# Kernel optimization log

Hardware: AMD Instinct MI355X
Metric: run time of the kernel (lower is better)

The kernel has to match this reference:

```python
import jax, jax.numpy as jnp
import numpy as np

B, H, W, C, WS, NCLS = 8, 256, 256, 256, 8, 18


def setup_inputs() -> dict:
    key = jax.random.key(0)
    ks = jax.random.split(key, 10)
    s = 1.0 / np.sqrt(C)
    return {
        "x": jax.random.normal(ks[0], (B, H, W, C), jnp.float32),
        "Wq": jax.random.normal(ks[1], (C, NCLS), jnp.float32) * s,
        "bq": jnp.zeros((NCLS,), jnp.float32),
        "Wk": jax.random.normal(ks[2], (C, NCLS), jnp.float32) * s,
        "bk": jnp.zeros((NCLS,), jnp.float32),
        "Wv": jax.random.normal(ks[3], (C, C), jnp.float32) * s,
        "bv": jnp.zeros((C,), jnp.float32),
        "Wres": jax.random.normal(ks[4], (C, C), jnp.float32) * s,
        "bres": jnp.zeros((C,), jnp.float32),
        "gamma": jnp.zeros((1,), jnp.float32) + 0.1,
    }


def _window_partition(x):
    # (B,H,W,C) -> (B*nH*nW, ws*ws, C)
    b, h, w, c = x.shape
    x = x.reshape(b, h // WS, WS, w // WS, WS, c)
    x = jnp.transpose(x, (0, 1, 3, 2, 4, 5))
    return x.reshape(-1, WS * WS, c)


def _window_reverse(xw, c):
    # (B*nH*nW, ws*ws, c) -> (B,H,W,c)
    x = xw.reshape(B, H // WS, W // WS, WS, WS, c)
    x = jnp.transpose(x, (0, 1, 3, 2, 4, 5))
    return x.reshape(B, H, W, c)


def reference(x, Wq, bq, Wk, bk, Wv, bv, Wres, bres, gamma):
    xw = _window_partition(x)                      # (nWin, ws^2, C)
    seg_map = xw @ Wq + bq                         # (nWin, ws^2, n_cls)
    seg_ft = xw @ Wk + bk                          # (nWin, ws^2, n_cls)
    feats = xw @ Wv + bv                           # (nWin, ws^2, C)
    score = jnp.einsum('nik,njk->nij', seg_map, seg_ft)  # (nWin, ws^2, ws^2)
    score = jax.nn.softmax(score, axis=-1)
    feats = jnp.einsum('nij,njc->nic', score, feats)
    feats = feats @ Wres + bres                    # dropout = identity (eval)
    feat_map = gamma * feats + xw
    return _window_reverse(seg_map, NCLS), _window_reverse(feat_map, C)
```

## Files before the change

### kernel.cpp

```cpp
#include <hip/hip_runtime.h>
#include <hip/hip_bf16.h>


typedef __bf16 bf16_t;
typedef __bf16 bf16x8 __attribute__((ext_vector_type(8)));
typedef __bf16 bf16x4 __attribute__((ext_vector_type(4)));
typedef float  f32x4  __attribute__((ext_vector_type(4)));

#define MFMA16(a, b, c) __builtin_amdgcn_mfma_f32_16x16x32_bf16((a), (b), (c), 0, 0, 0)

static constexpr int kC = 256, kNCLS = 18;
static constexpr int WQT_OFF = 0;
static constexpr int WKT_OFF = 8192;
static constexpr int WFT_OFF = 16384;
static constexpr int BF_BYTE_OFF = 81920 * 2;

__global__ __launch_bounds__(256) void prep_kernel(
    const float* __restrict__ Wq, const float* __restrict__ Wk,
    const float* __restrict__ Wv, const float* __restrict__ bv,
    const float* __restrict__ Wres, const float* __restrict__ bres,
    bf16_t* __restrict__ wsb, float* __restrict__ bff)
{
  const int blk = blockIdx.x, t = threadIdx.x;
  if (blk < 256) {
    __shared__ float wcol[256];
    const int n = blk;
    wcol[t] = Wres[t * kC + n];
    __syncthreads();
    float acc = 0.f;
    const float* wvrow = Wv + (size_t)t * kC;
#pragma unroll 4
    for (int j = 0; j < 256; j += 4) {
      f32x4 a = *(const f32x4*)(wvrow + j);
      acc += a[0] * wcol[j] + a[1] * wcol[j + 1] + a[2] * wcol[j + 2] + a[3] * wcol[j + 3];
    }
    wsb[WFT_OFF + n * kC + t] = (bf16_t)acc;
  } else if (blk == 256) {
    float acc = bres[t];
    for (int j = 0; j < 256; ++j) acc += bv[j] * Wres[j * kC + t];
    bff[t] = acc;
  } else {
    int tid = (blk - 257) * 256 + t;
    if (tid < 8192) {
      int n = tid >> 8, k = tid & 255;
      wsb[WQT_OFF + tid] = (n < kNCLS) ? (bf16_t)Wq[k * kNCLS + n] : (bf16_t)0.0f;
    } else {
      int u = tid - 8192;
      int n = u >> 8, k = u & 255;
      wsb[WKT_OFF + u] = (n < kNCLS) ? (bf16_t)Wk[k * kNCLS + n] : (bf16_t)0.0f;
    }
  }
}

__global__ __launch_bounds__(256, 3) void semwin_main(
    const float* __restrict__ x,
    const float* __restrict__ bq, const float* __restrict__ bk,
    const float* __restrict__ gamma,
    const bf16_t* __restrict__ wsb, const float* __restrict__ bff,
    float* __restrict__ out0, float* __restrict__ out1)
{
  __shared__ bf16_t xs[64][264];
  __shared__ __align__(16) char buf1[10240];
  __shared__ __align__(16) char buf2[9216];

  bf16_t (* const Qs)[40]  = (bf16_t(*)[40])(buf1);
  bf16_t (* const Ks)[40]  = (bf16_t(*)[40])(buf1 + 5120);
  bf16_t (* const Ps)[72]  = (bf16_t(*)[72])(buf1);
  bf16_t (* const Utc)[72] = (bf16_t(*)[72])(buf2);

  const int tid  = threadIdx.x;
  const int wave = tid >> 6;
  const int lane = tid & 63;
  const int l15  = lane & 15;
  const int g    = lane >> 4;

  const int wid = blockIdx.x;
  const int b   = wid >> 10;
  const int wh  = (wid >> 5) & 31;
  const int ww  = wid & 31;
  const int pixbase = (b << 16) + (wh << 11) + (ww << 3);

  const f32x4 fzero = {0.f, 0.f, 0.f, 0.f};
  const float gm = gamma[0];

  {
    const int t = tid >> 2;
    const int q = tid & 3;
    const float* src = x + (size_t)(pixbase + ((t >> 3) << 8) + (t & 7)) * kC + q * 8;
#pragma unroll
    for (int i = 0; i < 8; ++i) {
      f32x4 a = *(const f32x4*)(src + i * 32);
      f32x4 c = *(const f32x4*)(src + i * 32 + 4);
      bf16x8 v;
      v[0] = (bf16_t)a[0]; v[1] = (bf16_t)a[1]; v[2] = (bf16_t)a[2]; v[3] = (bf16_t)a[3];
      v[4] = (bf16_t)c[0]; v[5] = (bf16_t)c[1]; v[6] = (bf16_t)c[2]; v[7] = (bf16_t)c[3];
      *(bf16x8*)&xs[t][i * 32 + q * 8] = v;
    }
  }
  __syncthreads();

  {
    const bf16_t* wt   = wsb + ((wave < 2) ? WQT_OFF : WKT_OFF);
    const float*  bias = (wave < 2) ? bq : bk;
    const int mbase = (wave & 1) << 5;
    f32x4 acc[2][2];
#pragma unroll
    for (int mt = 0; mt < 2; ++mt)
#pragma unroll
      for (int nt = 0; nt < 2; ++nt) acc[mt][nt] = fzero;
#pragma unroll
    for (int k0 = 0; k0 < 256; k0 += 32) {
      bf16x8 a0 = *(const bf16x8*)&xs[mbase + l15][k0 + g * 8];
      bf16x8 a1 = *(const bf16x8*)&xs[mbase + 16 + l15][k0 + g * 8];
      bf16x8 b0 = *(const bf16x8*)(wt + l15 * 256 + k0 + g * 8);
      bf16x8 b1 = *(const bf16x8*)(wt + (16 + l15) * 256 + k0 + g * 8);
      acc[0][0] = MFMA16(a0, b0, acc[0][0]);
      acc[0][1] = MFMA16(a0, b1, acc[0][1]);
      acc[1][0] = MFMA16(a1, b0, acc[1][0]);
      acc[1][1] = MFMA16(a1, b1, acc[1][1]);
    }
    bf16_t (* const dst)[40] = (wave < 2) ? Qs : Ks;
    const bool isQ = (wave < 2);
#pragma unroll
    for (int nt = 0; nt < 2; ++nt) {
      const int coln = (nt << 4) + l15;
      const float bval = (coln < kNCLS) ? bias[coln] : 0.f;
#pragma unroll
      for (int mt = 0; mt < 2; ++mt) {
#pragma unroll
        for (int r = 0; r < 4; ++r) {
          const int row = mbase + (mt << 4) + (g << 2) + r;
          const float v = acc[mt][nt][r] + bval;
          dst[row][coln] = (bf16_t)v;
          if (isQ && coln < kNCLS) {
            out0[(size_t)(pixbase + ((row >> 3) << 8) + (row & 7)) * kNCLS + coln] = v;
          }
        }
      }
    }
  }
  __syncthreads();

  {
    const int mbase = wave << 4;
    const bf16x8 aq = *(const bf16x8*)&Qs[mbase + l15][g * 8];
    f32x4 s[4];
#pragma unroll
    for (int nt = 0; nt < 4; ++nt) {
      bf16x8 bk8 = *(const bf16x8*)&Ks[(nt << 4) + l15][g * 8];
      s[nt] = MFMA16(aq, bk8, fzero);
    }
    __syncthreads();
#pragma unroll
    for (int r = 0; r < 4; ++r) {
      float m = fmaxf(fmaxf(s[0][r], s[1][r]), fmaxf(s[2][r], s[3][r]));
#pragma unroll
      for (int off = 1; off < 16; off <<= 1) m = fmaxf(m, __shfl_xor(m, off));
      float e0 = __expf(s[0][r] - m), e1 = __expf(s[1][r] - m);
      float e2 = __expf(s[2][r] - m), e3 = __expf(s[3][r] - m);
      float sum = (e0 + e1) + (e2 + e3);
#pragma unroll
      for (int off = 1; off < 16; off <<= 1) sum += __shfl_xor(sum, off);
      const float inv = 1.0f / sum;
      const int row = mbase + (g << 2) + r;
      Ps[row][l15]      = (bf16_t)(e0 * inv);
      Ps[row][16 + l15] = (bf16_t)(e1 * inv);
      Ps[row][32 + l15] = (bf16_t)(e2 * inv);
      Ps[row][48 + l15] = (bf16_t)(e3 * inv);
    }
  }
  __syncthreads();

  bf16x8 bp[4][2];
#pragma unroll
  for (int nt = 0; nt < 4; ++nt) {
    bp[nt][0] = *(const bf16x8*)&Ps[(nt << 4) + l15][g * 8];
    bp[nt][1] = *(const bf16x8*)&Ps[(nt << 4) + l15][32 + g * 8];
  }

  for (int chunk = 0; chunk < 4; ++chunk) {
    {
      const bf16_t* wft = wsb + WFT_OFF + (size_t)((chunk << 6) + (wave << 4)) * 256;
      f32x4 accV[4];
#pragma unroll
      for (int mt = 0; mt < 4; ++mt) accV[mt] = fzero;
#pragma unroll
      for (int k0 = 0; k0 < 256; k0 += 32) {
        bf16x8 bf = *(const bf16x8*)(wft + l15 * 256 + k0 + g * 8);
#pragma unroll
        for (int mt = 0; mt < 4; ++mt) {
          bf16x8 af = *(const bf16x8*)&xs[(mt << 4) + l15][k0 + g * 8];
          accV[mt] = MFMA16(af, bf, accV[mt]);
        }
      }
#pragma unroll
      for (int mt = 0; mt < 4; ++mt) {
        bf16x4 pk;
#pragma unroll
        for (int r = 0; r < 4; ++r) pk[r] = (bf16_t)accV[mt][r];
        *(bf16x4*)&Utc[(wave << 4) + l15][(mt << 4) + (g << 2)] = pk;
      }
    }
    __syncthreads();

    {
      const bf16x8 av0 = *(const bf16x8*)&Utc[(wave << 4) + l15][g * 8];
      const bf16x8 av1 = *(const bf16x8*)&Utc[(wave << 4) + l15][32 + g * 8];
      const int c2 = (chunk << 6) + (wave << 4) + (g << 2);
      const f32x4 bfv = *(const f32x4*)(bff + c2);
#pragma unroll
      for (int nt = 0; nt < 4; ++nt) {
        f32x4 accC = MFMA16(av0, bp[nt][0], fzero);
        accC = MFMA16(av1, bp[nt][1], accC);
        const int t = (nt << 4) + l15;
        const bf16x4 xv = *(const bf16x4*)&xs[t][c2];
        f32x4 o;
#pragma unroll
        for (int r = 0; r < 4; ++r)
          o[r] = gm * (accC[r] + bfv[r]) + (float)xv[r];
        *(f32x4*)(out1 + (size_t)(pixbase + ((t >> 3) << 8) + (t & 7)) * kC + c2) = o;
      }
    }
    if (chunk < 3) __syncthreads();
  }
}

extern "C" void kernel_launch(void* const* d_in, const int* in_sizes, int n_in,
                              void* d_out, int out_size, void* d_ws, size_t ws_size,
                              hipStream_t stream)
{
  const float* x     = (const float*)d_in[0];
  const float* Wq    = (const float*)d_in[1];
  const float* bq    = (const float*)d_in[2];
  const float* Wk    = (const float*)d_in[3];
  const float* bk    = (const float*)d_in[4];
  const float* Wv    = (const float*)d_in[5];
  const float* bv    = (const float*)d_in[6];
  const float* Wres  = (const float*)d_in[7];
  const float* bres  = (const float*)d_in[8];
  const float* gamma = (const float*)d_in[9];
  bf16_t* wsb = (bf16_t*)d_ws;
  float*  bff = (float*)((char*)d_ws + BF_BYTE_OFF);
  float* out0 = (float*)d_out;
  float* out1 = out0 + (size_t)8 * 256 * 256 * 18;

  prep_kernel<<<dim3(321), dim3(256), 0, stream>>>(Wq, Wk, Wv, bv, Wres, bres, wsb, bff);
  semwin_main<<<dim3(8192), dim3(256), 0, stream>>>(x, bq, bk, gamma, wsb, bff, out0, out1);
}
```

Measured before the change: 324.2 us.

## Shrink LDS with XOR-swizzled unpadded buffers, alias scratch, raise occupancy to 4

Replaces the padded shared-memory arrays with unpadded XOR-swizzled layouts and folds the Q/K, P and U scratch into a single 64x64 buffer. This cuts LDS per block from about 53KB to 40KB, so launch bounds can ask for 4 blocks per CU instead of 3. Barriers become a raw LDS waitcnt plus s_barrier, which avoids waiting on outstanding global stores. An extra barrier is added after the P fragments are read, since the buffer is now reused for U. The risks are tighter register limits at 4 waves per SIMD and possible bank conflicts from the swizzle on some access patterns.

```diff
diff --git a/kernel.cpp b/kernel.cpp
--- a/kernel.cpp
+++ b/kernel.cpp
@@ -8,12 +8,17 @@
 typedef float  f32x4  __attribute__((ext_vector_type(4)));
 
 #define MFMA16(a, b, c) __builtin_amdgcn_mfma_f32_16x16x32_bf16((a), (b), (c), 0, 0, 0)
+#define BAR() do { asm volatile("s_waitcnt lgkmcnt(0)" ::: "memory"); \
+                   __builtin_amdgcn_s_barrier(); } while (0)
 
 static constexpr int kC = 256, kNCLS = 18;
 static constexpr int WQT_OFF = 0;
 static constexpr int WKT_OFF = 8192;
 static constexpr int WFT_OFF = 16384;
 static constexpr int BF_BYTE_OFF = 81920 * 2;
+
+__device__ __forceinline__ int xs_i(int r, int c) { return (r << 8) + (c ^ ((r & 7) << 3)); }
+__device__ __forceinline__ int sb_i(int r, int c) { return (r << 6) + (c ^ ((r & 7) << 3)); }
 
 __global__ __launch_bounds__(256) void prep_kernel(
     const float* __restrict__ Wq, const float* __restrict__ Wk,
@@ -52,21 +57,15 @@
   }
 }
 
-__global__ __launch_bounds__(256, 3) void semwin_main(
+__global__ __launch_bounds__(256, 4) void semwin_main(
     const float* __restrict__ x,
     const float* __restrict__ bq, const float* __restrict__ bk,
     const float* __restrict__ gamma,
     const bf16_t* __restrict__ wsb, const float* __restrict__ bff,
     float* __restrict__ out0, float* __restrict__ out1)
 {
-  __shared__ bf16_t xs[64][264];
-  __shared__ __align__(16) char buf1[10240];
-  __shared__ __align__(16) char buf2[9216];
-
-  bf16_t (* const Qs)[40]  = (bf16_t(*)[40])(buf1);
-  bf16_t (* const Ks)[40]  = (bf16_t(*)[40])(buf1 + 5120);
-  bf16_t (* const Ps)[72]  = (bf16_t(*)[72])(buf1);
-  bf16_t (* const Utc)[72] = (bf16_t(*)[72])(buf2);
+  __shared__ bf16_t xsf[64 * 256];
+  __shared__ bf16_t sbf[64 * 64];
 
   const int tid  = threadIdx.x;
   const int wave = tid >> 6;
@@ -94,15 +93,16 @@
       bf16x8 v;
       v[0] = (bf16_t)a[0]; v[1] = (bf16_t)a[1]; v[2] = (bf16_t)a[2]; v[3] = (bf16_t)a[3];
       v[4] = (bf16_t)c[0]; v[5] = (bf16_t)c[1]; v[6] = (bf16_t)c[2]; v[7] = (bf16_t)c[3];
-      *(bf16x8*)&xs[t][i * 32 + q * 8] = v;
-    }
-  }
-  __syncthreads();
+      *(bf16x8*)&xsf[xs_i(t, i * 32 + q * 8)] = v;
+    }
+  }
+  BAR();
 
   {
     const bf16_t* wt   = wsb + ((wave < 2) ? WQT_OFF : WKT_OFF);
     const float*  bias = (wave < 2) ? bq : bk;
     const int mbase = (wave & 1) << 5;
+    const int cofs  = (wave < 2) ? 0 : 32;
     f32x4 acc[2][2];
 #pragma unroll
     for (int mt = 0; mt < 2; ++mt)
@@ -110,8 +110,8 @@
       for (int nt = 0; nt < 2; ++nt) acc[mt][nt] = fzero;
 #pragma unroll
     for (int k0 = 0; k0 < 256; k0 += 32) {
-      bf16x8 a0 = *(const bf16x8*)&xs[mbase + l15][k0 + g * 8];
-      bf16x8 a1 = *(const bf16x8*)&xs[mbase + 16 + l15][k0 + g * 8];
+      bf16x8 a0 = *(const bf16x8*)&xsf[xs_i(mbase + l15, k0 + g * 8)];
+      bf16x8 a1 = *(const bf16x8*)&xsf[xs_i(mbase + 16 + l15, k0 + g * 8)];
       bf16x8 b0 = *(const bf16x8*)(wt + l15 * 256 + k0 + g * 8);
       bf16x8 b1 = *(const bf16x8*)(wt + (16 + l15) * 256 + k0 + g * 8);
       acc[0][0] = MFMA16(a0, b0, acc[0][0]);
@@ -119,7 +119,6 @@
       acc[1][0] = MFMA16(a1, b0, acc[1][0]);
       acc[1][1] = MFMA16(a1, b1, acc[1][1]);
     }
-    bf16_t (* const dst)[40] = (wave < 2) ? Qs : Ks;
     const bool isQ = (wave < 2);
 #pragma unroll
     for (int nt = 0; nt < 2; ++nt) {
@@ -131,7 +130,7 @@
         for (int r = 0; r < 4; ++r) {
           const int row = mbase + (mt << 4) + (g << 2) + r;
           const float v = acc[mt][nt][r] + bval;
-          dst[row][coln] = (bf16_t)v;
+          sbf[sb_i(row, cofs + coln)] = (bf16_t)v;
           if (isQ && coln < kNCLS) {
             out0[(size_t)(pixbase + ((row >> 3) << 8) + (row & 7)) * kNCLS + coln] = v;
           }
@@ -139,18 +138,18 @@
       }
     }
   }
-  __syncthreads();
+  BAR();
 
   {
     const int mbase = wave << 4;
-    const bf16x8 aq = *(const bf16x8*)&Qs[mbase + l15][g * 8];
+    const bf16x8 aq = *(const bf16x8*)&sbf[sb_i(mbase + l15, g * 8)];
     f32x4 s[4];
 #pragma unroll
     for (int nt = 0; nt < 4; ++nt) {
-      bf16x8 bk8 = *(const bf16x8*)&Ks[(nt << 4) + l15][g * 8];
+      bf16x8 bk8 = *(const bf16x8*)&sbf[sb_i((nt << 4) + l15, 32 + g * 8)];
       s[nt] = MFMA16(aq, bk8, fzero);
     }
-    __syncthreads();
+    BAR();
 #pragma unroll
     for (int r = 0; r < 4; ++r) {
       float m = fmaxf(fmaxf(s[0][r], s[1][r]), fmaxf(s[2][r], s[3][r]));
@@ -163,20 +162,21 @@
       for (int off = 1; off < 16; off <<= 1) sum += __shfl_xor(sum, off);
       const float inv = 1.0f / sum;
       const int row = mbase + (g << 2) + r;
-      Ps[row][l15]      = (bf16_t)(e0 * inv);
-      Ps[row][16 + l15] = (bf16_t)(e1 * inv);
-      Ps[row][32 + l15] = (bf16_t)(e2 * inv);
-      Ps[row][48 + l15] = (bf16_t)(e3 * inv);
-    }
-  }
-  __syncthreads();
+      sbf[sb_i(row, l15)]      = (bf16_t)(e0 * inv);
+      sbf[sb_i(row, 16 + l15)] = (bf16_t)(e1 * inv);
+      sbf[sb_i(row, 32 + l15)] = (bf16_t)(e2 * inv);
+      sbf[sb_i(row, 48 + l15)] = (bf16_t)(e3 * inv);
+    }
+  }
+  BAR();
 
   bf16x8 bp[4][2];
 #pragma unroll
   for (int nt = 0; nt < 4; ++nt) {
-    bp[nt][0] = *(const bf16x8*)&Ps[(nt << 4) + l15][g * 8];
-    bp[nt][1] = *(const bf16x8*)&Ps[(nt << 4) + l15][32 + g * 8];
-  }
+    bp[nt][0] = *(const bf16x8*)&sbf[sb_i((nt << 4) + l15, g * 8)];
+    bp[nt][1] = *(const bf16x8*)&sbf[sb_i((nt << 4) + l15, 32 + g * 8)];
+  }
+  BAR();
 
   for (int chunk = 0; chunk < 4; ++chunk) {
     {
@@ -189,7 +189,7 @@
         bf16x8 bf = *(const bf16x8*)(wft + l15 * 256 + k0 + g * 8);
 #pragma unroll
         for (int mt = 0; mt < 4; ++mt) {
-          bf16x8 af = *(const bf16x8*)&xs[(mt << 4) + l15][k0 + g * 8];
+          bf16x8 af = *(const bf16x8*)&xsf[xs_i((mt << 4) + l15, k0 + g * 8)];
           accV[mt] = MFMA16(af, bf, accV[mt]);
         }
       }
@@ -198,14 +198,14 @@
         bf16x4 pk;
 #pragma unroll
         for (int r = 0; r < 4; ++r) pk[r] = (bf16_t)accV[mt][r];
-        *(bf16x4*)&Utc[(wave << 4) + l15][(mt << 4) + (g << 2)] = pk;
-      }
-    }
-    __syncthreads();
+        *(bf16x4*)&sbf[sb_i((wave << 4) + l15, (mt << 4) + (g << 2))] = pk;
+      }
+    }
+    BAR();
 
     {
-      const bf16x8 av0 = *(const bf16x8*)&Utc[(wave << 4) + l15][g * 8];
-      const bf16x8 av1 = *(const bf16x8*)&Utc[(wave << 4) + l15][32 + g * 8];
+      const bf16x8 av0 = *(const bf16x8*)&sbf[sb_i((wave << 4) + l15, g * 8)];
+      const bf16x8 av1 = *(const bf16x8*)&sbf[sb_i((wave << 4) + l15, 32 + g * 8)];
       const int c2 = (chunk << 6) + (wave << 4) + (g << 2);
       const f32x4 bfv = *(const f32x4*)(bff + c2);
 #pragma unroll
@@ -213,7 +213,7 @@
         f32x4 accC = MFMA16(av0, bp[nt][0], fzero);
         accC = MFMA16(av1, bp[nt][1], accC);
         const int t = (nt << 4) + l15;
-        const bf16x4 xv = *(const bf16x4*)&xs[t][c2];
+        const bf16x4 xv = *(const bf16x4*)&xsf[xs_i(t, c2)];
         f32x4 o;
 #pragma unroll
         for (int r = 0; r < 4; ++r)
@@ -221,7 +221,7 @@
         *(f32x4*)(out1 + (size_t)(pixbase + ((t >> 3) << 8) + (t & 7)) * kC + c2) = o;
       }
     }
-    if (chunk < 3) __syncthreads();
+    if (chunk < 3) BAR();
   }
 }
 
```

Measured after the change: 315.8 us. 1.03x faster.
